# Performance work log

Measured on AMD Instinct MI355X. Metric: run time of the kernel, lower is better.

## Reference

```python
import jax, jax.numpy as jnp
import numpy as np

EPS = 1e-5
NUM_HEADS = 12

def _ln(x, g, b):
    m = jnp.mean(x, -1, keepdims=True)
    v = jnp.var(x, -1, keepdims=True)
    return (x - m) * jax.lax.rsqrt(v + EPS) * g + b

def setup_inputs():
    key = jax.random.key(0)
    ks = jax.random.split(key, 8)
    D, Dh = 768, 3072
    B, T, H, Wd = 8, 8, 14, 14
    def w(k, shape, scale=0.02):
        return jax.random.normal(k, shape, jnp.float32) * scale
    return dict(
        x=jax.random.normal(ks[0], (B, T * H * Wd + 1, D), jnp.float32),
        W_mq=w(ks[1], (D, D)), b_mq=jnp.zeros((D,), jnp.float32),
        W_mk=w(ks[2], (D, D)), b_mk=jnp.zeros((D,), jnp.float32),
        g1=jnp.ones((D,), jnp.float32), be1=jnp.zeros((D,), jnp.float32),
        W_qkv=w(ks[3], (3 * D, D)),
        W_proj=w(ks[4], (D, D)), b_proj=jnp.zeros((D,), jnp.float32),
        g2=jnp.ones((D,), jnp.float32), be2=jnp.zeros((D,), jnp.float32),
        W_fc1=w(ks[5], (Dh, D)), b_fc1=jnp.zeros((Dh,), jnp.float32),
        W_fc2=w(ks[6], (D, Dh)), b_fc2=jnp.zeros((D,), jnp.float32),
        B=B, T=T, H=H, Wd=Wd,
    )

def reference(x, W_mq, b_mq, W_mk, b_mk, g1, be1, W_qkv, W_proj, b_proj,
              g2, be2, W_fc1, b_fc1, W_fc2, b_fc2, B, T, H, Wd):
    D = x.shape[-1]
    nh = NUM_HEADS
    hd = D // nh
    res = x
    # cls token: (B,1,D) -> repeated per frame -> (B*T,1,D)
    cls = jnp.repeat(x[:, :1, :], T, axis=1).reshape(B * T, 1, D)
    # spatial tokens: 'b (h w t) m -> (b t) (h w) m'  (t is fastest-varying)
    xs = x[:, 1:, :].reshape(B, H * Wd, T, D).transpose(0, 2, 1, 3).reshape(B * T, H * Wd, D)
    xt = jnp.concatenate([cls, xs], axis=1)  # (BT, N=197, D)
    # learned QK-gated mask
    qm = xt @ W_mq.T + b_mq
    km = xt @ W_mk.T + b_mk
    lm = jnp.einsum('bnd,bmd->bnm', qm, km)
    lm = lm.at[:, 0, 0].set(100.0)  # force cls->cls gate open
    lm = jax.nn.sigmoid(lm)
    # attention (drop rates are 0; drop_path is identity at inference)
    xn = _ln(xt, g1, be1)
    BT, N = xt.shape[0], xt.shape[1]
    qkv = (xn @ W_qkv.T).reshape(BT, N, 3, nh, hd).transpose(2, 0, 3, 1, 4)
    q, k, v = qkv[0], qkv[1], qkv[2]  # (BT, nh, N, hd)
    attn = jax.nn.softmax(jnp.einsum('bhnd,bhmd->bhnm', q, k) * (hd ** -0.5), axis=-1)
    attn = attn * lm[:, None, :, :]  # gate attention probs with learned mask
    o = jnp.einsum('bhnm,bhmd->bhnd', attn, v).transpose(0, 2, 1, 3).reshape(BT, N, D)
    o = o @ W_proj.T + b_proj
    # gather cls back (mean over frames) and scatter tokens back
    cls_o = jnp.mean(o[:, 0, :].reshape(B, T, D), axis=1, keepdims=True)  # (B,1,D)
    xs_o = o[:, 1:, :].reshape(B, T, H * Wd, D).transpose(0, 2, 1, 3).reshape(B, H * Wd * T, D)
    y = res + jnp.concatenate([cls_o, xs_o], axis=1)
    # MLP
    h = _ln(y, g2, be2)
    h = jax.nn.gelu(h @ W_fc1.T + b_fc1, approximate=False)
    y = y + (h @ W_fc2.T + b_fc2)
    return (y, lm)
```

## Files before the change

kernel.cpp:

```cpp
#include <hip/hip_runtime.h>
#include <cstdint>

typedef _Float16 f16;
typedef f16 f16x2 __attribute__((ext_vector_type(2)));
typedef f16 f16x4 __attribute__((ext_vector_type(4)));
typedef f16 f16x8 __attribute__((ext_vector_type(8)));
typedef float f32x4 __attribute__((ext_vector_type(4)));

constexpr int D = 768;
constexpr int NTOK = 197;
constexpr int BT = 64;
constexpr int ROWS_A = BT * NTOK;
constexpr int SEQ = 1569;
constexpr int ROWS_Y = 8 * SEQ;
constexpr int DH = 3072;
constexpr int CW = 2304;
constexpr long Y_ELEMS = (long)ROWS_Y * D;

__device__ __forceinline__ void gload_lds16(const f16* g, f16* l) {
  __builtin_amdgcn_global_load_lds(
      (const __attribute__((address_space(1))) void*)g,
      (__attribute__((address_space(3))) void*)l, 16, 0, 0);
}

constexpr int DD4 = D * D / 4;
constexpr int QKV4 = CW * D / 4;
constexpr int FC4 = DH * D / 4;
constexpr int WQ_TOT = 3 * DD4 + QKV4 + 2 * FC4;

__global__ __launch_bounds__(256) void cvt_weights(
    const float* __restrict__ wmq_f, const float* __restrict__ wmk_f,
    const float* __restrict__ wqkv_f, const float* __restrict__ wproj_f,
    const float* __restrict__ wfc1_f, const float* __restrict__ wfc2_f,
    f16* __restrict__ wmqk, f16* __restrict__ wqkv, f16* __restrict__ wproj,
    f16* __restrict__ wfc1, f16* __restrict__ wfc2) {
  const int i = blockIdx.x * 256 + threadIdx.x;
  const float* src;
  f16* dst;
  int j;
  if (i < DD4) { src = wmq_f; dst = wmqk; j = i; }
  else if (i < 2 * DD4) { src = wmk_f; dst = wmqk + (size_t)D * D; j = i - DD4; }
  else if (i < 2 * DD4 + QKV4) { src = wqkv_f; dst = wqkv; j = i - 2 * DD4; }
  else if (i < 3 * DD4 + QKV4) { src = wproj_f; dst = wproj; j = i - 2 * DD4 - QKV4; }
  else if (i < 3 * DD4 + QKV4 + FC4) { src = wfc1_f; dst = wfc1; j = i - 3 * DD4 - QKV4; }
  else if (i < WQ_TOT) { src = wfc2_f; dst = wfc2; j = i - 3 * DD4 - QKV4 - FC4; }
  else return;
  const float4 v = *(const float4*)(src + (size_t)j * 4);
  f16x4 o = {(f16)v.x, (f16)v.y, (f16)v.z, (f16)v.w};
  *(f16x4*)(dst + (size_t)j * 4) = o;
}

__global__ __launch_bounds__(256) void concat2_f32(const float* __restrict__ a,
                                                   const float* __restrict__ b,
                                                   float* __restrict__ o, int n) {
  int i = blockIdx.x * 256 + threadIdx.x;
  if (i < n) o[i] = a[i];
  else if (i < 2 * n) o[i] = b[i - n];
}

__global__ __launch_bounds__(192) void build_xt_xn(
    const float* __restrict__ x, const float* __restrict__ g1,
    const float* __restrict__ be1, f16* __restrict__ xt, f16* __restrict__ xn) {
  const int rid = blockIdx.x;
  const int bt = rid / NTOK, n = rid % NTOK;
  const int b = bt >> 3, t = bt & 7;
  const int src = (n == 0) ? b * SEQ : b * SEQ + 1 + (n - 1) * 8 + t;
  const int tid = threadIdx.x, d0 = tid * 4;
  const float4 v = *(const float4*)(x + (size_t)src * D + d0);
  float s = v.x + v.y + v.z + v.w;
  float q = v.x * v.x + v.y * v.y + v.z * v.z + v.w * v.w;
  const int lane = tid & 63, wv = tid >> 6;
  for (int off = 32; off; off >>= 1) {
    s += __shfl_xor(s, off);
    q += __shfl_xor(q, off);
  }
  __shared__ float red[2][3];
  if (lane == 0) { red[0][wv] = s; red[1][wv] = q; }
  __syncthreads();
  s = red[0][0] + red[0][1] + red[0][2];
  q = red[1][0] + red[1][1] + red[1][2];
  const float mean = s * (1.f / 768.f);
  const float var = q * (1.f / 768.f) - mean * mean;
  const float rs = rsqrtf(var + 1e-5f);
  const size_t ob = (size_t)rid * D + d0;
  f16x4 xo = {(f16)v.x, (f16)v.y, (f16)v.z, (f16)v.w};
  *(f16x4*)(xt + ob) = xo;
  const float4 gv = *(const float4*)(g1 + d0);
  const float4 bv = *(const float4*)(be1 + d0);
  f16x4 no = {(f16)((v.x - mean) * rs * gv.x + bv.x),
              (f16)((v.y - mean) * rs * gv.y + bv.y),
              (f16)((v.z - mean) * rs * gv.z + bv.z),
              (f16)((v.w - mean) * rs * gv.w + bv.w)};
  *(f16x4*)(xn + ob) = no;
}

constexpr int EPI_F16 = 0;
constexpr int EPI_F16_BIAS = 1;
constexpr int EPI_SIG = 2;
constexpr int EPI_F16_BIAS_GELU = 3;
constexpr int EPI_F32_BIAS_RES = 4;
constexpr int EPI_F32_ATOMIC = 5;

template <int EPI>
__global__ __launch_bounds__(256, 3) void gemm_f16(
    const f16* __restrict__ A, const f16* __restrict__ B,
    const float* __restrict__ bias, float* __restrict__ Cf,
    f16* __restrict__ Ch, const float* __restrict__ Res, int M, int N, int K,
    int lda, int ldb, int ldc, long sA, long sB, long sC) {
  constexpr int BM = 128, BN = 128, BK = 32;
  __shared__ f16 As[3][BM][BK];
  __shared__ f16 Bs[3][BN][BK];
  const int tid = threadIdx.x;
  const int bm = blockIdx.y * BM, bn = blockIdx.x * BN;
  const int z = blockIdx.z;
  A += (size_t)z * sA;
  B += (size_t)z * sB;
  const int lane = tid & 63, wave = tid >> 6;
  const int wm = (wave >> 1) * 64, wn = (wave & 1) * 64;
  const int l15 = lane & 15, quad = lane >> 4;

  const int gr = lane >> 2;
  const int gc = (lane & 3) * 8;
  int a_row0 = bm + wave * 16 + gr;       if (a_row0 >= M) a_row0 = M - 1;
  int a_row1 = bm + (wave + 4) * 16 + gr; if (a_row1 >= M) a_row1 = M - 1;
  int b_row0 = bn + wave * 16 + gr;       if (b_row0 >= N) b_row0 = N - 1;
  int b_row1 = bn + (wave + 4) * 16 + gr; if (b_row1 >= N) b_row1 = N - 1;
  const f16* ap0 = A + (size_t)a_row0 * lda + gc;
  const f16* ap1 = A + (size_t)a_row1 * lda + gc;
  const f16* bp0 = B + (size_t)b_row0 * ldb + gc;
  const f16* bp1 = B + (size_t)b_row1 * ldb + gc;

  f32x4 acc[4][4] = {};

  auto stage = [&](int buf, int k) {
    gload_lds16(ap0 + k, &As[buf][wave * 16][0]);
    gload_lds16(ap1 + k, &As[buf][(wave + 4) * 16][0]);
    gload_lds16(bp0 + k, &Bs[buf][wave * 16][0]);
    gload_lds16(bp1 + k, &Bs[buf][(wave + 4) * 16][0]);
  };
  auto compute = [&](int buf) {
    f16x8 af[4], bf[4];
#pragma unroll
    for (int i = 0; i < 4; i++) {
      af[i] = *(const f16x8*)&As[buf][wm + i * 16 + l15][quad * 8];
      bf[i] = *(const f16x8*)&Bs[buf][wn + i * 16 + l15][quad * 8];
    }
#pragma unroll
    for (int i = 0; i < 4; i++)
#pragma unroll
      for (int j = 0; j < 4; j++)
        acc[i][j] =
            __builtin_amdgcn_mfma_f32_16x16x32_f16(af[i], bf[j], acc[i][j], 0, 0, 0);
  };

  const int NT = K / BK;
  stage(0, 0);
  stage(1, BK);
  for (int kt = 0; kt < NT - 1; ++kt) {
    asm volatile("s_waitcnt vmcnt(4)" ::: "memory");
    __builtin_amdgcn_sched_barrier(0);
    __builtin_amdgcn_s_barrier();
    __builtin_amdgcn_sched_barrier(0);
    if (kt + 2 < NT) stage((kt + 2) % 3, (kt + 2) * BK);
    compute(kt % 3);
  }
  asm volatile("s_waitcnt vmcnt(0)" ::: "memory");
  __builtin_amdgcn_sched_barrier(0);
  __builtin_amdgcn_s_barrier();
  __builtin_amdgcn_sched_barrier(0);
  compute((NT - 1) % 3);

#pragma unroll
  for (int i = 0; i < 4; i++) {
#pragma unroll
    for (int j = 0; j < 4; j++) {
      const int col = bn + wn + j * 16 + l15;
      if (col >= N) continue;
#pragma unroll
      for (int r = 0; r < 4; r++) {
        const int row = bm + wm + i * 16 + quad * 4 + r;
        if (row >= M) continue;
        float v = acc[i][j][r];
        const size_t ci = (size_t)z * sC + (size_t)row * ldc + col;
        if constexpr (EPI == EPI_F16) {
          Ch[ci] = (f16)v;
        } else if constexpr (EPI == EPI_F16_BIAS) {
          Ch[ci] = (f16)(v + bias[col]);
        } else if constexpr (EPI == EPI_SIG) {
          if (row == 0 && col == 0) v = 100.f;
          Cf[ci] = 1.f / (1.f + __expf(-v));
        } else if constexpr (EPI == EPI_F16_BIAS_GELU) {
          const float u = v + bias[col];
          const float t = u * (0.79788456f + 0.0356774081f * u * u);
          const float e = __expf(2.f * t);
          Ch[ci] = (f16)(u * (e / (e + 1.f)));
        } else if constexpr (EPI == EPI_F32_BIAS_RES) {
          Cf[ci] = v + bias[col] + Res[ci];
        } else if constexpr (EPI == EPI_F32_ATOMIC) {
          atomicAdd(Cf + ci, v);
        }
      }
    }
  }
}

__global__ __launch_bounds__(256, 2) void attn_kernel(
    const f16* __restrict__ qkv, const float* __restrict__ lm,
    f16* __restrict__ o) {
  __shared__ f16 Ks[208][72];
  __shared__ f16 Vt[64][232];
  __shared__ f16 Ps[4][16][40];
  const int bh = blockIdx.x;
  const int bt = bh / 12, h = bh % 12;
  const int tid = threadIdx.x, lane = tid & 63, w = tid >> 6;
  const int l15 = lane & 15, quad = lane >> 4;
  const size_t base = (size_t)bt * NTOK * CW + (size_t)h * 64;

  for (int idx = tid; idx < 208 * 8; idx += 256) {
    const int r = idx >> 3, c = (idx & 7) * 8;
    f16x8 kv = {};
    if (r < NTOK) kv = *(const f16x8*)(qkv + base + (size_t)r * CW + 768 + c);
    *(f16x8*)&Ks[r][c] = kv;
  }
  for (int cb = 0; cb < 8; cb++) {
    const int r = tid;
    if (r < NTOK) {
      const f16x8 vv = *(const f16x8*)(qkv + base + (size_t)r * CW + 1536 + cb * 8);
#pragma unroll
      for (int j = 0; j < 8; j++) Vt[cb * 8 + j][r] = vv[j];
    }
  }
  for (int idx = tid; idx < 64 * 35; idx += 256) {
    const int d = idx / 35, m = NTOK + idx % 35;
    Vt[d][m] = (f16)0.f;
  }
  __syncthreads();

  for (int nt = w; nt < 13; nt += 4) {
    const int nq = nt * 16 + l15;
    const f16* qrow = qkv + base + (size_t)nq * CW;
    const f16x8 aq0 = *(const f16x8*)(qrow + quad * 8);
    const f16x8 aq1 = *(const f16x8*)(qrow + 32 + quad * 8);
    f32x4 S[13];
#pragma unroll
    for (int t = 0; t < 13; t++) {
      const f16x8 bk0 = *(const f16x8*)&Ks[t * 16 + l15][quad * 8];
      const f16x8 bk1 = *(const f16x8*)&Ks[t * 16 + l15][32 + quad * 8];
      f32x4 s = {};
      s = __builtin_amdgcn_mfma_f32_16x16x32_f16(aq0, bk0, s, 0, 0, 0);
      s = __builtin_amdgcn_mfma_f32_16x16x32_f16(aq1, bk1, s, 0, 0, 0);
      S[t] = s;
    }
    float mx[4] = {-3e38f, -3e38f, -3e38f, -3e38f};
#pragma unroll
    for (int t = 0; t < 13; t++) {
      const int m = t * 16 + l15;
#pragma unroll
      for (int r = 0; r < 4; r++) {
        float v = (m < NTOK) ? S[t][r] * 0.125f : -1e30f;
        S[t][r] = v;
        mx[r] = fmaxf(mx[r], v);
      }
    }
#pragma unroll
    for (int off = 1; off < 16; off <<= 1)
#pragma unroll
      for (int r = 0; r < 4; r++) mx[r] = fmaxf(mx[r], __shfl_xor(mx[r], off));
    float den[4] = {0.f, 0.f, 0.f, 0.f};
#pragma unroll
    for (int t = 0; t < 13; t++)
#pragma unroll
      for (int r = 0; r < 4; r++) {
        const float e = __expf(S[t][r] - mx[r]);
        S[t][r] = e;
        den[r] += e;
      }
#pragma unroll
    for (int off = 1; off < 16; off <<= 1)
#pragma unroll
      for (int r = 0; r < 4; r++) den[r] += __shfl_xor(den[r], off);
    float inv[4];
#pragma unroll
    for (int r = 0; r < 4; r++) inv[r] = 1.f / den[r];
#pragma unroll
    for (int t = 0; t < 13; t++) {
      const int m = t * 16 + l15;
#pragma unroll
      for (int r = 0; r < 4; r++) {
        const int nrow = nt * 16 + quad * 4 + r;
        float g = 0.f;
        if (m < NTOK && nrow < NTOK)
          g = lm[((size_t)bt * NTOK + nrow) * NTOK + m];
        S[t][r] *= inv[r] * g;
      }
    }
    f32x4 O[4] = {};
    for (int c = 0; c < 7; c++) {
      __builtin_amdgcn_wave_barrier();
#pragma unroll
      for (int tt = 0; tt < 2; tt++) {
        const int t = 2 * c + tt;
#pragma unroll
        for (int r = 0; r < 4; r++) {
          const f16 pv = (t < 13) ? (f16)S[t][r] : (f16)0.f;
          Ps[w][quad * 4 + r][tt * 16 + l15] = pv;
        }
      }
      __builtin_amdgcn_wave_barrier();
      const f16x8 ap = *(const f16x8*)&Ps[w][l15][quad * 8];
#pragma unroll
      for (int dt = 0; dt < 4; dt++) {
        const f16x8 bv = *(const f16x8*)&Vt[dt * 16 + l15][c * 32 + quad * 8];
        O[dt] = __builtin_amdgcn_mfma_f32_16x16x32_f16(ap, bv, O[dt], 0, 0, 0);
      }
    }
#pragma unroll
    for (int dt = 0; dt < 4; dt++)
#pragma unroll
      for (int r = 0; r < 4; r++) {
        const int nrow = nt * 16 + quad * 4 + r;
        if (nrow < NTOK)
          o[((size_t)bt * NTOK + nrow) * D + h * 64 + dt * 16 + l15] =
              (f16)O[dt][r];
      }
  }
}

__global__ __launch_bounds__(192) void scatter_y_ln(
    const float* __restrict__ x, const f16* __restrict__ po,
    const float* __restrict__ g2, const float* __restrict__ be2,
    const float* __restrict__ bfc2,
    float* __restrict__ y, f16* __restrict__ yn) {
  const int rid = blockIdx.x;
  const int b = rid / SEQ, pos = rid % SEQ;
  const int tid = threadIdx.x, d0 = tid * 4;
  float4 v = *(const float4*)(x + (size_t)rid * D + d0);
  if (pos == 0) {
    float ax = 0, ay = 0, az = 0, aw = 0;
    for (int t = 0; t < 8; t++) {
      const f16x4 p = *(const f16x4*)(po + ((size_t)(b * 8 + t) * NTOK) * D + d0);
      ax += (float)p[0]; ay += (float)p[1]; az += (float)p[2]; aw += (float)p[3];
    }
    v.x += ax * 0.125f; v.y += ay * 0.125f; v.z += az * 0.125f; v.w += aw * 0.125f;
  } else {
    const int hw = (pos - 1) >> 3, t = (pos - 1) & 7;
    const f16x4 p =
        *(const f16x4*)(po + ((size_t)((b * 8 + t) * NTOK + 1 + hw)) * D + d0);
    v.x += (float)p[0]; v.y += (float)p[1]; v.z += (float)p[2]; v.w += (float)p[3];
  }
  const float4 b2 = *(const float4*)(bfc2 + d0);
  float4 vo = {v.x + b2.x, v.y + b2.y, v.z + b2.z, v.w + b2.w};
  *(float4*)(y + (size_t)rid * D + d0) = vo;
  float s = v.x + v.y + v.z + v.w;
  float q = v.x * v.x + v.y * v.y + v.z * v.z + v.w * v.w;
  const int lane = tid & 63, wv = tid >> 6;
  for (int off = 32; off; off >>= 1) {
    s += __shfl_xor(s, off);
    q += __shfl_xor(q, off);
  }
  __shared__ float red[2][3];
  if (lane == 0) { red[0][wv] = s; red[1][wv] = q; }
  __syncthreads();
  s = red[0][0] + red[0][1] + red[0][2];
  q = red[1][0] + red[1][1] + red[1][2];
  const float mean = s * (1.f / 768.f);
  const float var = q * (1.f / 768.f) - mean * mean;
  const float rs = rsqrtf(var + 1e-5f);
  const float4 gv = *(const float4*)(g2 + d0);
  const float4 bv = *(const float4*)(be2 + d0);
  f16x4 no = {(f16)((v.x - mean) * rs * gv.x + bv.x),
              (f16)((v.y - mean) * rs * gv.y + bv.y),
              (f16)((v.z - mean) * rs * gv.z + bv.z),
              (f16)((v.w - mean) * rs * gv.w + bv.w)};
  *(f16x4*)(yn + (size_t)rid * D + d0) = no;
}

extern "C" void kernel_launch(void* const* d_in, const int* in_sizes, int n_in,
                              void* d_out, int out_size, void* d_ws,
                              size_t ws_size, hipStream_t stream) {
  const float* x = (const float*)d_in[0];
  const float* W_mq = (const float*)d_in[1];
  const float* b_mq = (const float*)d_in[2];
  const float* W_mk = (const float*)d_in[3];
  const float* b_mk = (const float*)d_in[4];
  const float* g1 = (const float*)d_in[5];
  const float* be1 = (const float*)d_in[6];
  const float* W_qkv = (const float*)d_in[7];
  const float* W_proj = (const float*)d_in[8];
  const float* b_proj = (const float*)d_in[9];
  const float* g2 = (const float*)d_in[10];
  const float* be2 = (const float*)d_in[11];
  const float* W_fc1 = (const float*)d_in[12];
  const float* b_fc1 = (const float*)d_in[13];
  const float* W_fc2 = (const float*)d_in[14];
  const float* b_fc2 = (const float*)d_in[15];

  char* ws = (char*)d_ws;
  size_t off = 0;
  auto alloc = [&](size_t bytes) {
    size_t o = off;
    off = (off + bytes + 255) & ~(size_t)255;
    return o;
  };
  const size_t o_wmqk = alloc((size_t)2 * D * D * 2);
  const size_t o_bmqk = alloc((size_t)2 * D * 4);
  const size_t o_wqkv = alloc((size_t)CW * D * 2);
  const size_t o_wproj = alloc((size_t)D * D * 2);
  const size_t o_wfc1 = alloc((size_t)DH * D * 2);
  const size_t o_wfc2 = alloc((size_t)D * DH * 2);
  const size_t o_xt = alloc((size_t)ROWS_A * D * 2);
  const size_t o_xn = alloc((size_t)ROWS_A * D * 2);
  const size_t o_big = alloc((size_t)ROWS_A * CW * 2);
  const size_t o_po = alloc((size_t)ROWS_A * D * 2);
  const size_t o_qmkm = o_big;
  const size_t o_qkv = o_big;
  const size_t o_o = o_xn;
  const size_t o_yn = o_xt;
  const size_t o_h = o_big;

  f16* wmqk = (f16*)(ws + o_wmqk);
  float* bmqk = (float*)(ws + o_bmqk);
  f16* wqkv = (f16*)(ws + o_wqkv);
  f16* wproj = (f16*)(ws + o_wproj);
  f16* wfc1 = (f16*)(ws + o_wfc1);
  f16* wfc2 = (f16*)(ws + o_wfc2);
  f16* xt = (f16*)(ws + o_xt);
  f16* xn = (f16*)(ws + o_xn);
  f16* qmkm = (f16*)(ws + o_qmkm);
  f16* qkv = (f16*)(ws + o_qkv);
  f16* oatt = (f16*)(ws + o_o);
  f16* po = (f16*)(ws + o_po);
  f16* yn = (f16*)(ws + o_yn);
  f16* h = (f16*)(ws + o_h);

  float* y_out = (float*)d_out;
  float* lm_out = (float*)d_out + Y_ELEMS;

  const dim3 blk(256);
  cvt_weights<<<dim3((WQ_TOT + 255) / 256), blk, 0, stream>>>(
      W_mq, W_mk, W_qkv, W_proj, W_fc1, W_fc2, wmqk, wqkv, wproj, wfc1, wfc2);
  concat2_f32<<<dim3(6), blk, 0, stream>>>(b_mq, b_mk, bmqk, D);

  build_xt_xn<<<dim3(ROWS_A), dim3(192), 0, stream>>>(x, g1, be1, xt, xn);

  auto grd = [](int N_, int M_, int Z_) {
    return dim3((N_ + 127) / 128, (M_ + 127) / 128, Z_);
  };
  gemm_f16<EPI_F16_BIAS><<<grd(2 * D, ROWS_A, 1), blk, 0, stream>>>(
      xt, wmqk, bmqk, nullptr, qmkm, nullptr, ROWS_A, 2 * D, D, D, D, 2 * D,
      0, 0, 0);
  gemm_f16<EPI_SIG><<<grd(NTOK, NTOK, BT), blk, 0, stream>>>(
      qmkm, qmkm + D, nullptr, lm_out, nullptr, nullptr, NTOK, NTOK, D,
      2 * D, 2 * D, NTOK, (long)NTOK * 2 * D, (long)NTOK * 2 * D,
      (long)NTOK * NTOK);
  gemm_f16<EPI_F16><<<grd(CW, ROWS_A, 1), blk, 0, stream>>>(
      xn, wqkv, nullptr, nullptr, qkv, nullptr, ROWS_A, CW, D, D, D, CW,
      0, 0, 0);
  attn_kernel<<<dim3(BT * 12), blk, 0, stream>>>(qkv, lm_out, oatt);
  gemm_f16<EPI_F16_BIAS><<<grd(D, ROWS_A, 1), blk, 0, stream>>>(
      oatt, wproj, b_proj, nullptr, po, nullptr, ROWS_A, D, D, D, D, D,
      0, 0, 0);
  scatter_y_ln<<<dim3(ROWS_Y), dim3(192), 0, stream>>>(x, po, g2, be2, b_fc2,
                                                       y_out, yn);
  gemm_f16<EPI_F16_BIAS_GELU><<<grd(DH, ROWS_Y, 1), blk, 0, stream>>>(
      yn, wfc1, b_fc1, nullptr, h, nullptr, ROWS_Y, DH, D, D, D, DH, 0, 0, 0);
  gemm_f16<EPI_F32_ATOMIC><<<grd(D, ROWS_Y, 2), blk, 0, stream>>>(
      h, wfc2, nullptr, y_out, nullptr, nullptr, ROWS_Y, D, 1536, DH, DH, D,
      1536, 1536, 0);
  (void)in_sizes; (void)n_in; (void)out_size; (void)ws_size;
}
```

Before: 677.1 us.

## Switch GEMM to double-buffered LDS and split-K the projection GEMM

Replaces the triple-buffered vmcnt-driven GEMM pipeline with a simpler two-buffer loop using block barriers, reducing LDS per block to allow more resident blocks. Splits the attention output projection into two K halves written as separate f16 partials, and folds the partial sum and projection bias into the scatter/LayerNorm kernel. This trades prefetch depth and extra barriers for occupancy, and adds partial-buffer traffic for more parallelism in the projection GEMM.

```diff
diff --git a/kernel.cpp b/kernel.cpp
--- a/kernel.cpp
+++ b/kernel.cpp
@@ -108,8 +108,8 @@
     f16* __restrict__ Ch, const float* __restrict__ Res, int M, int N, int K,
     int lda, int ldb, int ldc, long sA, long sB, long sC) {
   constexpr int BM = 128, BN = 128, BK = 32;
-  __shared__ f16 As[3][BM][BK];
-  __shared__ f16 Bs[3][BN][BK];
+  __shared__ f16 As[2][BM][BK];
+  __shared__ f16 Bs[2][BN][BK];
   const int tid = threadIdx.x;
   const int bm = blockIdx.y * BM, bn = blockIdx.x * BN;
   const int z = blockIdx.z;
@@ -153,22 +153,16 @@
             __builtin_amdgcn_mfma_f32_16x16x32_f16(af[i], bf[j], acc[i][j], 0, 0, 0);
   };
 
-  const int NT = K / BK;
   stage(0, 0);
-  stage(1, BK);
-  for (int kt = 0; kt < NT - 1; ++kt) {
-    asm volatile("s_waitcnt vmcnt(4)" ::: "memory");
-    __builtin_amdgcn_sched_barrier(0);
-    __builtin_amdgcn_s_barrier();
-    __builtin_amdgcn_sched_barrier(0);
-    if (kt + 2 < NT) stage((kt + 2) % 3, (kt + 2) * BK);
-    compute(kt % 3);
-  }
-  asm volatile("s_waitcnt vmcnt(0)" ::: "memory");
-  __builtin_amdgcn_sched_barrier(0);
-  __builtin_amdgcn_s_barrier();
-  __builtin_amdgcn_sched_barrier(0);
-  compute((NT - 1) % 3);
+  __syncthreads();
+  for (int kt = 0; kt < K; kt += 2 * BK) {
+    stage(1, kt + BK);
+    compute(0);
+    __syncthreads();
+    if (kt + 2 * BK < K) stage(0, kt + 2 * BK);
+    compute(1);
+    __syncthreads();
+  }
 
 #pragma unroll
   for (int i = 0; i < 4; i++) {
@@ -327,7 +321,8 @@
 }
 
 __global__ __launch_bounds__(192) void scatter_y_ln(
-    const float* __restrict__ x, const f16* __restrict__ po,
+    const float* __restrict__ x, const f16* __restrict__ po0,
+    const f16* __restrict__ po1, const float* __restrict__ bpj,
     const float* __restrict__ g2, const float* __restrict__ be2,
     const float* __restrict__ bfc2,
     float* __restrict__ y, f16* __restrict__ yn) {
@@ -335,18 +330,27 @@
   const int b = rid / SEQ, pos = rid % SEQ;
   const int tid = threadIdx.x, d0 = tid * 4;
   float4 v = *(const float4*)(x + (size_t)rid * D + d0);
+  const float4 bp = *(const float4*)(bpj + d0);
   if (pos == 0) {
     float ax = 0, ay = 0, az = 0, aw = 0;
     for (int t = 0; t < 8; t++) {
-      const f16x4 p = *(const f16x4*)(po + ((size_t)(b * 8 + t) * NTOK) * D + d0);
-      ax += (float)p[0]; ay += (float)p[1]; az += (float)p[2]; aw += (float)p[3];
-    }
-    v.x += ax * 0.125f; v.y += ay * 0.125f; v.z += az * 0.125f; v.w += aw * 0.125f;
+      const size_t pi = ((size_t)(b * 8 + t) * NTOK) * D + d0;
+      const f16x4 p = *(const f16x4*)(po0 + pi);
+      const f16x4 q = *(const f16x4*)(po1 + pi);
+      ax += (float)p[0] + (float)q[0]; ay += (float)p[1] + (float)q[1];
+      az += (float)p[2] + (float)q[2]; aw += (float)p[3] + (float)q[3];
+    }
+    v.x += ax * 0.125f + bp.x; v.y += ay * 0.125f + bp.y;
+    v.z += az * 0.125f + bp.z; v.w += aw * 0.125f + bp.w;
   } else {
     const int hw = (pos - 1) >> 3, t = (pos - 1) & 7;
-    const f16x4 p =
-        *(const f16x4*)(po + ((size_t)((b * 8 + t) * NTOK + 1 + hw)) * D + d0);
-    v.x += (float)p[0]; v.y += (float)p[1]; v.z += (float)p[2]; v.w += (float)p[3];
+    const size_t pi = ((size_t)((b * 8 + t) * NTOK + 1 + hw)) * D + d0;
+    const f16x4 p = *(const f16x4*)(po0 + pi);
+    const f16x4 q = *(const f16x4*)(po1 + pi);
+    v.x += (float)p[0] + (float)q[0] + bp.x;
+    v.y += (float)p[1] + (float)q[1] + bp.y;
+    v.z += (float)p[2] + (float)q[2] + bp.z;
+    v.w += (float)p[3] + (float)q[3] + bp.w;
   }
   const float4 b2 = *(const float4*)(bfc2 + d0);
   float4 vo = {v.x + b2.x, v.y + b2.y, v.z + b2.z, v.w + b2.w};
@@ -411,10 +415,11 @@
   const size_t o_xt = alloc((size_t)ROWS_A * D * 2);
   const size_t o_xn = alloc((size_t)ROWS_A * D * 2);
   const size_t o_big = alloc((size_t)ROWS_A * CW * 2);
-  const size_t o_po = alloc((size_t)ROWS_A * D * 2);
+  const size_t o_spare = alloc((size_t)ROWS_A * D * 2);
   const size_t o_qmkm = o_big;
   const size_t o_qkv = o_big;
   const size_t o_o = o_xn;
+  const size_t o_po = o_big;
   const size_t o_yn = o_xt;
   const size_t o_h = o_big;
 
@@ -429,9 +434,10 @@
   f16* qmkm = (f16*)(ws + o_qmkm);
   f16* qkv = (f16*)(ws + o_qkv);
   f16* oatt = (f16*)(ws + o_o);
-  f16* po = (f16*)(ws + o_po);
+  f16* po01 = (f16*)(ws + o_po);
   f16* yn = (f16*)(ws + o_yn);
   f16* h = (f16*)(ws + o_h);
+  (void)o_spare;
 
   float* y_out = (float*)d_out;
   float* lm_out = (float*)d_out + Y_ELEMS;
@@ -457,11 +463,11 @@
       xn, wqkv, nullptr, nullptr, qkv, nullptr, ROWS_A, CW, D, D, D, CW,
       0, 0, 0);
   attn_kernel<<<dim3(BT * 12), blk, 0, stream>>>(qkv, lm_out, oatt);
-  gemm_f16<EPI_F16_BIAS><<<grd(D, ROWS_A, 1), blk, 0, stream>>>(
-      oatt, wproj, b_proj, nullptr, po, nullptr, ROWS_A, D, D, D, D, D,
-      0, 0, 0);
-  scatter_y_ln<<<dim3(ROWS_Y), dim3(192), 0, stream>>>(x, po, g2, be2, b_fc2,
-                                                       y_out, yn);
+  gemm_f16<EPI_F16><<<grd(D, ROWS_A, 2), blk, 0, stream>>>(
+      oatt, wproj, nullptr, nullptr, po01, nullptr, ROWS_A, D, 384, D, D, D,
+      384, 384, (long)ROWS_A * D);
+  scatter_y_ln<<<dim3(ROWS_Y), dim3(192), 0, stream>>>(
+      x, po01, po01 + (size_t)ROWS_A * D, b_proj, g2, be2, b_fc2, y_out, yn);
   gemm_f16<EPI_F16_BIAS_GELU><<<grd(DH, ROWS_Y, 1), blk, 0, stream>>>(
       yn, wfc1, b_fc1, nullptr, h, nullptr, ROWS_Y, DH, D, D, D, DH, 0, 0, 0);
   gemm_f16<EPI_F32_ATOMIC><<<grd(D, ROWS_Y, 2), blk, 0, stream>>>(
```

After: 680.2 us. Within noise of the previous version (+0.5%).
